# Performance work log

Measured on AMD Instinct MI355X. Metric: run time of the kernel, lower is better.

## Reference

```python
import jax, jax.numpy as jnp
import numpy as np

NUM_HEAD = 16

def setup_inputs() -> dict:
    rk = jax.random.key(0)
    k1, k2, k3, k4, k5 = jax.random.split(rk, 5)
    B, Sq, Skv, D = 4, 2048, 2048, 1024
    return {
        "query": jax.random.normal(k1, (B, Sq, D), dtype=jnp.float32),
        "key":   jax.random.normal(k2, (B, Skv, D), dtype=jnp.float32),
        "value": jax.random.normal(k3, (B, Skv, D), dtype=jnp.float32),
        "W": jax.random.normal(k4, (D, D), dtype=jnp.float32) * (D ** -0.5),
        "b": jax.random.normal(k5, (D,), dtype=jnp.float32) * 0.01,
    }

def reference(query, key, value, W, b):
    B, Sq, D = query.shape
    H = NUM_HEAD
    hd = D // H
    # chunk(num_head, -1) == split last dim into H contiguous heads
    q = query.reshape(B, Sq, H, hd)
    k = key.reshape(B, -1, H, hd)
    v = value.reshape(B, -1, H, hd)
    # scores[b,h,q,k] = (Q_h K_h^T) / sqrt(embedding_dim)  (full dim, per source)
    scores = jnp.einsum('bqhd,bkhd->bhqk', q, k) / jnp.sqrt(jnp.float32(D))
    # nn.Softmax(dim=1) on a [B, q, kv] matrix -> softmax over the QUERY axis
    attn = jax.nn.softmax(scores, axis=2)
    out = jnp.einsum('bhqk,bkhd->bqhd', attn, v).reshape(B, Sq, D)
    # final linear: x @ W^T + b
    return out @ W.T + b
```

## Files before the change

kernel.cpp:

```cpp
#include <hip/hip_runtime.h>

#define NH    16
#define HD    64
#define SQ    2048
#define SKV   2048
#define DM    1024

typedef __attribute__((ext_vector_type(8))) __bf16 bf16x8;
typedef __attribute__((ext_vector_type(4))) __bf16 bf16x4;
typedef __attribute__((ext_vector_type(4))) float  f32x4;

#define ASYNC16(gp, lp)                                                        \
    __builtin_amdgcn_global_load_lds(                                          \
        (const __attribute__((address_space(1))) void*)(gp),                   \
        (__attribute__((address_space(3))) void*)(lp), 16, 0, 0)

#if __has_builtin(__builtin_amdgcn_exp2f)
#define EXPS(x) __builtin_amdgcn_exp2f((x) * 0.04508422f)
#else
#define EXPS(x) __expf((x) * 0.03125f)
#endif

static __device__ __forceinline__ int swz(int row, int chunk) {
    return (row << 6) + (((chunk) ^ (row & 7)) << 3);
}

static __device__ __forceinline__ bf16x4 cvt4(float4 v) {
    bf16x4 r;
    r[0] = (__bf16)v.x; r[1] = (__bf16)v.y; r[2] = (__bf16)v.z; r[3] = (__bf16)v.w;
    return r;
}

__global__ void kprep(const float* __restrict__ src, __bf16* __restrict__ dst) {
    size_t g = (size_t)blockIdx.x * 256 + threadIdx.x;
    size_t o = g * 8;
    int c  = (int)(o & 63);
    int s  = (int)((o >> 6) & 2047);
    int bh = (int)(o >> 17);
    int b = bh >> 4, h = bh & 15;
    const float* p = src + ((size_t)(b * SQ + s)) * DM + h * HD + c;
    float4 v0 = *(const float4*)p;
    float4 v1 = *(const float4*)(p + 4);
    bf16x8 r;
    r[0] = (__bf16)v0.x; r[1] = (__bf16)v0.y; r[2] = (__bf16)v0.z; r[3] = (__bf16)v0.w;
    r[4] = (__bf16)v1.x; r[5] = (__bf16)v1.y; r[6] = (__bf16)v1.z; r[7] = (__bf16)v1.w;
    *(bf16x8*)(dst + o) = r;
}

__global__ void kconv_w(const float* __restrict__ W, __bf16* __restrict__ Wb) {
    int i = blockIdx.x * 256 + threadIdx.x;
    float4 v = *(const float4*)(W + (size_t)i * 4);
    *(bf16x4*)(Wb + (size_t)i * 4) = cvt4(v);
}

__global__ __launch_bounds__(256, 3) void kz(const __bf16* __restrict__ Qh,
                                             const __bf16* __restrict__ Kh,
                                             const float* __restrict__ v,
                                             __bf16* __restrict__ Vt) {
    const int bh = blockIdx.x;
    const int kb = blockIdx.y;
    const int b = bh >> 4, h = bh & 15;
    const int t = threadIdx.x;
    const int w = t >> 6, lane = t & 63;
    const int lo16 = lane & 15, quad = lane >> 4;
    const int wub = (t & 192) << 3;

    __shared__ __bf16 Ks[256 * 64];
    __shared__ __bf16 Qs[64 * 64];
    __shared__ float  Zs[256];

    const __bf16* kbase = Kh + ((size_t)bh * SKV + kb * 256) * HD;
    const __bf16* qbase = Qh + (size_t)bh * SQ * HD;

#pragma unroll
    for (int i = 0; i < 8; ++i) {
        int ci = i * 256 + t;
        int row = ci >> 3;
        int c = (ci & 7) ^ (row & 7);
        ASYNC16(kbase + row * 64 + c * 8, &Ks[i * 2048 + wub]);
    }
    __syncthreads();

    bf16x8 bk[4][2];
#pragma unroll
    for (int nt = 0; nt < 4; ++nt)
#pragma unroll
        for (int dh = 0; dh < 2; ++dh)
            bk[nt][dh] = *(const bf16x8*)(&Ks[swz(w * 64 + nt * 16 + lo16, dh * 4 + quad)]);

    float zacc[4] = {0.f, 0.f, 0.f, 0.f};

    for (int qt = 0; qt < 32; ++qt) {
        __syncthreads();
#pragma unroll
        for (int i = 0; i < 2; ++i) {
            int ci = i * 256 + t;
            int row = ci >> 3;
            int c = (ci & 7) ^ (row & 7);
            ASYNC16(qbase + (size_t)qt * 64 * HD + row * 64 + c * 8, &Qs[i * 2048 + wub]);
        }
        __syncthreads();

#pragma unroll
        for (int mt = 0; mt < 4; ++mt) {
            bf16x8 aq0 = *(const bf16x8*)(&Qs[swz(mt * 16 + lo16, quad)]);
            bf16x8 aq1 = *(const bf16x8*)(&Qs[swz(mt * 16 + lo16, 4 + quad)]);
#pragma unroll
            for (int nt = 0; nt < 4; ++nt) {
                f32x4 acc = {0.f, 0.f, 0.f, 0.f};
                acc = __builtin_amdgcn_mfma_f32_16x16x32_bf16(aq0, bk[nt][0], acc, 0, 0, 0);
                acc = __builtin_amdgcn_mfma_f32_16x16x32_bf16(aq1, bk[nt][1], acc, 0, 0, 0);
                zacc[nt] += EXPS(acc[0]) + EXPS(acc[1]) + EXPS(acc[2]) + EXPS(acc[3]);
            }
        }
    }

#pragma unroll
    for (int nt = 0; nt < 4; ++nt) {
        float s = zacc[nt];
        s += __shfl_xor(s, 16, 64);
        s += __shfl_xor(s, 32, 64);
        if (lane < 16) Zs[w * 64 + nt * 16 + lane] = s;
    }
    __syncthreads();

    {
        float rz = 1.0f / Zs[t];
        const float* vrow = v + ((size_t)(b * SKV) + kb * 256 + t) * DM + h * HD;
        size_t vtb = (size_t)bh * HD * SKV + kb * 256 + t;
#pragma unroll
        for (int dc = 0; dc < 4; ++dc) {
            float4 a0 = *(const float4*)(vrow + dc * 16 + 0);
            float4 a1 = *(const float4*)(vrow + dc * 16 + 4);
            float4 a2 = *(const float4*)(vrow + dc * 16 + 8);
            float4 a3 = *(const float4*)(vrow + dc * 16 + 12);
            float tmp[16] = {a0.x, a0.y, a0.z, a0.w, a1.x, a1.y, a1.z, a1.w,
                             a2.x, a2.y, a2.z, a2.w, a3.x, a3.y, a3.z, a3.w};
#pragma unroll
            for (int j = 0; j < 16; ++j)
                Vt[vtb + (size_t)(dc * 16 + j) * SKV] = (__bf16)(tmp[j] * rz);
        }
    }
}

__global__ __launch_bounds__(256, 3) void kattn(const __bf16* __restrict__ Qh,
                                                const __bf16* __restrict__ Kh,
                                                const __bf16* __restrict__ Vt,
                                                __bf16* __restrict__ O) {
    const int bh = blockIdx.x;
    const int qb = blockIdx.y;
    const int b = bh >> 4, h = bh & 15;
    const int t = threadIdx.x;
    const int w = t >> 6, lane = t & 63;
    const int lo16 = lane & 15, quad = lane >> 4;
    const int wub = (t & 192) << 3;

    __shared__ __bf16 Ks[64 * 64];
    __shared__ __bf16 Vts[64 * 64];
    __shared__ __bf16 QE[256 * 64];

    const __bf16* qgbase = Qh + ((size_t)bh * SQ + qb * 256) * HD;
#pragma unroll
    for (int i = 0; i < 8; ++i) {
        int ci = i * 256 + t;
        int row = ci >> 3;
        int c = (ci & 7) ^ (row & 7);
        ASYNC16(qgbase + row * 64 + c * 8, &QE[i * 2048 + wub]);
    }
    __syncthreads();

    bf16x8 qf[4][2];
#pragma unroll
    for (int qt = 0; qt < 4; ++qt)
#pragma unroll
        for (int dh = 0; dh < 2; ++dh)
            qf[qt][dh] = *(const bf16x8*)(&QE[swz(w * 64 + qt * 16 + lo16, dh * 4 + quad)]);

    f32x4 oacc[4][4];
    f32x4 zero = {0.f, 0.f, 0.f, 0.f};
#pragma unroll
    for (int qt = 0; qt < 4; ++qt)
#pragma unroll
        for (int nt = 0; nt < 4; ++nt)
            oacc[qt][nt] = zero;

    __bf16* Ew = &QE[w * 64 * 64];
    const __bf16* kgbase = Kh + (size_t)bh * SKV * HD;
    const __bf16* vtgbase = Vt + (size_t)bh * HD * SKV;

    for (int kt = 0; kt < 32; ++kt) {
        __syncthreads();
#pragma unroll
        for (int i = 0; i < 2; ++i) {
            int ci = i * 256 + t;
            int row = ci >> 3;
            int c = (ci & 7) ^ (row & 7);
            ASYNC16(kgbase + (size_t)kt * 64 * HD + row * 64 + c * 8, &Ks[i * 2048 + wub]);
            ASYNC16(vtgbase + (size_t)row * SKV + kt * 64 + c * 8, &Vts[i * 2048 + wub]);
        }
        __syncthreads();

#pragma unroll
        for (int ktile = 0; ktile < 4; ++ktile) {
            bf16x8 ak0 = *(const bf16x8*)(&Ks[swz(ktile * 16 + lo16, quad)]);
            bf16x8 ak1 = *(const bf16x8*)(&Ks[swz(ktile * 16 + lo16, 4 + quad)]);
#pragma unroll
            for (int qt = 0; qt < 4; ++qt) {
                f32x4 s = zero;
                s = __builtin_amdgcn_mfma_f32_16x16x32_bf16(ak0, qf[qt][0], s, 0, 0, 0);
                s = __builtin_amdgcn_mfma_f32_16x16x32_bf16(ak1, qf[qt][1], s, 0, 0, 0);
                bf16x4 e;
                e[0] = (__bf16)EXPS(s[0]);
                e[1] = (__bf16)EXPS(s[1]);
                e[2] = (__bf16)EXPS(s[2]);
                e[3] = (__bf16)EXPS(s[3]);
                int er = qt * 16 + lo16;
                *(bf16x4*)(&Ew[(er << 6) + ((((2 * ktile + (quad >> 1))) ^ (er & 7)) << 3)
                               + (quad & 1) * 4]) = e;
            }
        }

#pragma unroll
        for (int kk2 = 0; kk2 < 2; ++kk2) {
            bf16x8 ae[4];
#pragma unroll
            for (int qt = 0; qt < 4; ++qt)
                ae[qt] = *(const bf16x8*)(&Ew[swz(qt * 16 + lo16, kk2 * 4 + quad)]);
#pragma unroll
            for (int nt = 0; nt < 4; ++nt) {
                bf16x8 bv = *(const bf16x8*)(&Vts[swz(nt * 16 + lo16, kk2 * 4 + quad)]);
#pragma unroll
                for (int qt = 0; qt < 4; ++qt)
                    oacc[qt][nt] = __builtin_amdgcn_mfma_f32_16x16x32_bf16(ae[qt], bv, oacc[qt][nt], 0, 0, 0);
            }
        }
    }

    size_t obase = ((size_t)(b * SQ) + qb * 256 + w * 64) * DM + h * HD;
#pragma unroll
    for (int qt = 0; qt < 4; ++qt)
#pragma unroll
        for (int nt = 0; nt < 4; ++nt)
#pragma unroll
            for (int r = 0; r < 4; ++r)
                O[obase + (size_t)(qt * 16 + quad * 4 + r) * DM + nt * 16 + lo16] =
                    (__bf16)oacc[qt][nt][r];
}

__global__ __launch_bounds__(256, 3) void kproj(const __bf16* __restrict__ A,
                                                const __bf16* __restrict__ Wb,
                                                const float* __restrict__ bias,
                                                float* __restrict__ out) {
    const int nb = blockIdx.x;
    const int mb = blockIdx.y;
    const int t = threadIdx.x;
    const int w = t >> 6, lane = t & 63;
    const int lo16 = lane & 15, quad = lane >> 4;
    const int wm = w & 1, wn = w >> 1;
    const int wub = (t & 192) << 3;

    __shared__ __bf16 As[128 * 64];
    __shared__ __bf16 Bs[128 * 64];

    f32x4 acc[4][4];
    f32x4 zero = {0.f, 0.f, 0.f, 0.f};
#pragma unroll
    for (int mt = 0; mt < 4; ++mt)
#pragma unroll
        for (int nt = 0; nt < 4; ++nt)
            acc[mt][nt] = zero;

    const __bf16* abase = A + (size_t)(mb * 128) * DM;
    const __bf16* wbase = Wb + (size_t)(nb * 128) * DM;

    for (int kt = 0; kt < 16; ++kt) {
        __syncthreads();
#pragma unroll
        for (int i = 0; i < 4; ++i) {
            int ci = i * 256 + t;
            int row = ci >> 3;
            int c = (ci & 7) ^ (row & 7);
            ASYNC16(abase + (size_t)row * DM + kt * 64 + c * 8, &As[i * 2048 + wub]);
            ASYNC16(wbase + (size_t)row * DM + kt * 64 + c * 8, &Bs[i * 2048 + wub]);
        }
        __syncthreads();

#pragma unroll
        for (int ks = 0; ks < 2; ++ks) {
            bf16x8 av[4], bv[4];
#pragma unroll
            for (int mt = 0; mt < 4; ++mt)
                av[mt] = *(const bf16x8*)(&As[swz(wm * 64 + mt * 16 + lo16, ks * 4 + quad)]);
#pragma unroll
            for (int nt = 0; nt < 4; ++nt)
                bv[nt] = *(const bf16x8*)(&Bs[swz(wn * 64 + nt * 16 + lo16, ks * 4 + quad)]);
#pragma unroll
            for (int mt = 0; mt < 4; ++mt)
#pragma unroll
                for (int nt = 0; nt < 4; ++nt)
                    acc[mt][nt] = __builtin_amdgcn_mfma_f32_16x16x32_bf16(av[mt], bv[nt], acc[mt][nt], 0, 0, 0);
        }
    }

    const int col0 = nb * 128 + wn * 64;
    const int row0 = mb * 128 + wm * 64;
#pragma unroll
    for (int nt = 0; nt < 4; ++nt) {
        float bb = bias[col0 + nt * 16 + lo16];
#pragma unroll
        for (int mt = 0; mt < 4; ++mt)
#pragma unroll
            for (int r = 0; r < 4; ++r)
                out[(size_t)(row0 + mt * 16 + quad * 4 + r) * DM + col0 + nt * 16 + lo16] =
                    acc[mt][nt][r] + bb;
    }
}

extern "C" void kernel_launch(void* const* d_in, const int* in_sizes, int n_in,
                              void* d_out, int out_size, void* d_ws, size_t ws_size,
                              hipStream_t stream) {
    const float* q    = (const float*)d_in[0];
    const float* k    = (const float*)d_in[1];
    const float* v    = (const float*)d_in[2];
    const float* W    = (const float*)d_in[3];
    const float* bias = (const float*)d_in[4];
    float* out = (float*)d_out;

    char* ws = (char*)d_ws;
    __bf16* Qh = (__bf16*)ws;
    __bf16* Kh = (__bf16*)(ws + (16u << 20));
    __bf16* Vt = (__bf16*)(ws + (32u << 20));
    __bf16* Wb = (__bf16*)(ws + (48u << 20));
    __bf16* O  = (__bf16*)(ws + (50u << 20));

    kprep  <<<dim3(4096), 256, 0, stream>>>(q, Qh);
    kprep  <<<dim3(4096), 256, 0, stream>>>(k, Kh);
    kconv_w<<<dim3(1024), 256, 0, stream>>>(W, Wb);
    kz     <<<dim3(64, 8), 256, 0, stream>>>(Qh, Kh, v, Vt);
    kattn  <<<dim3(64, 8), 256, 0, stream>>>(Qh, Kh, Vt, O);
    kproj  <<<dim3(8, 64), 256, 0, stream>>>(O, Wb, bias, out);
}
```

Before: 298.5 us.

## Double-buffer LDS tiles in attention and projection kernels, merge prep launches

Switches the kz, kattn and kproj main loops from single-buffered LDS tiles to double buffering. The next tile's async global-to-LDS load is issued before computing on the current tile, with one barrier per iteration instead of two. The three conversion kernels are merged into one launch, and launch_bounds occupancy hints drop from 3 to 2 blocks per CU to make room for the larger shared footprint. The risk is lower occupancy, and the overlap depends on the async loads being waited on correctly at the single barrier.

```diff
diff --git a/kernel.cpp b/kernel.cpp
--- a/kernel.cpp
+++ b/kernel.cpp
@@ -31,29 +31,35 @@
     return r;
 }
 
-__global__ void kprep(const float* __restrict__ src, __bf16* __restrict__ dst) {
-    size_t g = (size_t)blockIdx.x * 256 + threadIdx.x;
-    size_t o = g * 8;
-    int c  = (int)(o & 63);
-    int s  = (int)((o >> 6) & 2047);
-    int bh = (int)(o >> 17);
-    int b = bh >> 4, h = bh & 15;
-    const float* p = src + ((size_t)(b * SQ + s)) * DM + h * HD + c;
-    float4 v0 = *(const float4*)p;
-    float4 v1 = *(const float4*)(p + 4);
-    bf16x8 r;
-    r[0] = (__bf16)v0.x; r[1] = (__bf16)v0.y; r[2] = (__bf16)v0.z; r[3] = (__bf16)v0.w;
-    r[4] = (__bf16)v1.x; r[5] = (__bf16)v1.y; r[6] = (__bf16)v1.z; r[7] = (__bf16)v1.w;
-    *(bf16x8*)(dst + o) = r;
-}
-
-__global__ void kconv_w(const float* __restrict__ W, __bf16* __restrict__ Wb) {
-    int i = blockIdx.x * 256 + threadIdx.x;
-    float4 v = *(const float4*)(W + (size_t)i * 4);
-    *(bf16x4*)(Wb + (size_t)i * 4) = cvt4(v);
-}
-
-__global__ __launch_bounds__(256, 3) void kz(const __bf16* __restrict__ Qh,
+__global__ void kprep_all(const float* __restrict__ q, const float* __restrict__ k,
+                          const float* __restrict__ W,
+                          __bf16* __restrict__ Qh, __bf16* __restrict__ Kh,
+                          __bf16* __restrict__ Wb) {
+    int bid = blockIdx.x;
+    if (bid < 8192) {
+        const float* src = (bid < 4096) ? q : k;
+        __bf16* dst = (bid < 4096) ? Qh : Kh;
+        size_t g = (size_t)(bid & 4095) * 256 + threadIdx.x;
+        size_t o = g * 8;
+        int c  = (int)(o & 63);
+        int s  = (int)((o >> 6) & 2047);
+        int bh = (int)(o >> 17);
+        int b = bh >> 4, h = bh & 15;
+        const float* p = src + ((size_t)(b * SQ + s)) * DM + h * HD + c;
+        float4 v0 = *(const float4*)p;
+        float4 v1 = *(const float4*)(p + 4);
+        bf16x8 r;
+        r[0] = (__bf16)v0.x; r[1] = (__bf16)v0.y; r[2] = (__bf16)v0.z; r[3] = (__bf16)v0.w;
+        r[4] = (__bf16)v1.x; r[5] = (__bf16)v1.y; r[6] = (__bf16)v1.z; r[7] = (__bf16)v1.w;
+        *(bf16x8*)(dst + o) = r;
+    } else {
+        int i = (bid - 8192) * 256 + threadIdx.x;
+        float4 v = *(const float4*)(W + (size_t)i * 4);
+        *(bf16x4*)(Wb + (size_t)i * 4) = cvt4(v);
+    }
+}
+
+__global__ __launch_bounds__(256, 2) void kz(const __bf16* __restrict__ Qh,
                                              const __bf16* __restrict__ Kh,
                                              const float* __restrict__ v,
                                              __bf16* __restrict__ Vt) {
@@ -66,7 +72,7 @@
     const int wub = (t & 192) << 3;
 
     __shared__ __bf16 Ks[256 * 64];
-    __shared__ __bf16 Qs[64 * 64];
+    __shared__ __bf16 Qs[2][64 * 64];
     __shared__ float  Zs[256];
 
     const __bf16* kbase = Kh + ((size_t)bh * SKV + kb * 256) * HD;
@@ -79,6 +85,13 @@
         int c = (ci & 7) ^ (row & 7);
         ASYNC16(kbase + row * 64 + c * 8, &Ks[i * 2048 + wub]);
     }
+#pragma unroll
+    for (int i = 0; i < 2; ++i) {
+        int ci = i * 256 + t;
+        int row = ci >> 3;
+        int c = (ci & 7) ^ (row & 7);
+        ASYNC16(qbase + row * 64 + c * 8, &Qs[0][i * 2048 + wub]);
+    }
     __syncthreads();
 
     bf16x8 bk[4][2];
@@ -91,20 +104,22 @@
     float zacc[4] = {0.f, 0.f, 0.f, 0.f};
 
     for (int qt = 0; qt < 32; ++qt) {
-        __syncthreads();
-#pragma unroll
-        for (int i = 0; i < 2; ++i) {
-            int ci = i * 256 + t;
-            int row = ci >> 3;
-            int c = (ci & 7) ^ (row & 7);
-            ASYNC16(qbase + (size_t)qt * 64 * HD + row * 64 + c * 8, &Qs[i * 2048 + wub]);
-        }
-        __syncthreads();
+        const int cur = qt & 1, nxt = cur ^ 1;
+        if (qt < 31) {
+#pragma unroll
+            for (int i = 0; i < 2; ++i) {
+                int ci = i * 256 + t;
+                int row = ci >> 3;
+                int c = (ci & 7) ^ (row & 7);
+                ASYNC16(qbase + (size_t)(qt + 1) * 64 * HD + row * 64 + c * 8,
+                        &Qs[nxt][i * 2048 + wub]);
+            }
+        }
 
 #pragma unroll
         for (int mt = 0; mt < 4; ++mt) {
-            bf16x8 aq0 = *(const bf16x8*)(&Qs[swz(mt * 16 + lo16, quad)]);
-            bf16x8 aq1 = *(const bf16x8*)(&Qs[swz(mt * 16 + lo16, 4 + quad)]);
+            bf16x8 aq0 = *(const bf16x8*)(&Qs[cur][swz(mt * 16 + lo16, quad)]);
+            bf16x8 aq1 = *(const bf16x8*)(&Qs[cur][swz(mt * 16 + lo16, 4 + quad)]);
 #pragma unroll
             for (int nt = 0; nt < 4; ++nt) {
                 f32x4 acc = {0.f, 0.f, 0.f, 0.f};
@@ -113,6 +128,7 @@
                 zacc[nt] += EXPS(acc[0]) + EXPS(acc[1]) + EXPS(acc[2]) + EXPS(acc[3]);
             }
         }
+        __syncthreads();
     }
 
 #pragma unroll
@@ -143,7 +159,7 @@
     }
 }
 
-__global__ __launch_bounds__(256, 3) void kattn(const __bf16* __restrict__ Qh,
+__global__ __launch_bounds__(256, 2) void kattn(const __bf16* __restrict__ Qh,
                                                 const __bf16* __restrict__ Kh,
                                                 const __bf16* __restrict__ Vt,
                                                 __bf16* __restrict__ O) {
@@ -155,17 +171,28 @@
     const int lo16 = lane & 15, quad = lane >> 4;
     const int wub = (t & 192) << 3;
 
-    __shared__ __bf16 Ks[64 * 64];
-    __shared__ __bf16 Vts[64 * 64];
+    __shared__ __bf16 Ks[2][64 * 64];
+    __shared__ __bf16 Vts[2][64 * 64];
     __shared__ __bf16 QE[256 * 64];
 
     const __bf16* qgbase = Qh + ((size_t)bh * SQ + qb * 256) * HD;
+    const __bf16* kgbase = Kh + (size_t)bh * SKV * HD;
+    const __bf16* vtgbase = Vt + (size_t)bh * HD * SKV;
+
 #pragma unroll
     for (int i = 0; i < 8; ++i) {
         int ci = i * 256 + t;
         int row = ci >> 3;
         int c = (ci & 7) ^ (row & 7);
         ASYNC16(qgbase + row * 64 + c * 8, &QE[i * 2048 + wub]);
+    }
+#pragma unroll
+    for (int i = 0; i < 2; ++i) {
+        int ci = i * 256 + t;
+        int row = ci >> 3;
+        int c = (ci & 7) ^ (row & 7);
+        ASYNC16(kgbase + row * 64 + c * 8, &Ks[0][i * 2048 + wub]);
+        ASYNC16(vtgbase + (size_t)row * SKV + c * 8, &Vts[0][i * 2048 + wub]);
     }
     __syncthreads();
 
@@ -185,25 +212,26 @@
             oacc[qt][nt] = zero;
 
     __bf16* Ew = &QE[w * 64 * 64];
-    const __bf16* kgbase = Kh + (size_t)bh * SKV * HD;
-    const __bf16* vtgbase = Vt + (size_t)bh * HD * SKV;
 
     for (int kt = 0; kt < 32; ++kt) {
-        __syncthreads();
-#pragma unroll
-        for (int i = 0; i < 2; ++i) {
-            int ci = i * 256 + t;
-            int row = ci >> 3;
-            int c = (ci & 7) ^ (row & 7);
-            ASYNC16(kgbase + (size_t)kt * 64 * HD + row * 64 + c * 8, &Ks[i * 2048 + wub]);
-            ASYNC16(vtgbase + (size_t)row * SKV + kt * 64 + c * 8, &Vts[i * 2048 + wub]);
-        }
-        __syncthreads();
+        const int cur = kt & 1, nxt = cur ^ 1;
+        if (kt < 31) {
+#pragma unroll
+            for (int i = 0; i < 2; ++i) {
+                int ci = i * 256 + t;
+                int row = ci >> 3;
+                int c = (ci & 7) ^ (row & 7);
+                ASYNC16(kgbase + (size_t)(kt + 1) * 64 * HD + row * 64 + c * 8,
+                        &Ks[nxt][i * 2048 + wub]);
+                ASYNC16(vtgbase + (size_t)row * SKV + (kt + 1) * 64 + c * 8,
+                        &Vts[nxt][i * 2048 + wub]);
+            }
+        }
 
 #pragma unroll
         for (int ktile = 0; ktile < 4; ++ktile) {
-            bf16x8 ak0 = *(const bf16x8*)(&Ks[swz(ktile * 16 + lo16, quad)]);
-            bf16x8 ak1 = *(const bf16x8*)(&Ks[swz(ktile * 16 + lo16, 4 + quad)]);
+            bf16x8 ak0 = *(const bf16x8*)(&Ks[cur][swz(ktile * 16 + lo16, quad)]);
+            bf16x8 ak1 = *(const bf16x8*)(&Ks[cur][swz(ktile * 16 + lo16, 4 + quad)]);
 #pragma unroll
             for (int qt = 0; qt < 4; ++qt) {
                 f32x4 s = zero;
@@ -228,12 +256,13 @@
                 ae[qt] = *(const bf16x8*)(&Ew[swz(qt * 16 + lo16, kk2 * 4 + quad)]);
 #pragma unroll
             for (int nt = 0; nt < 4; ++nt) {
-                bf16x8 bv = *(const bf16x8*)(&Vts[swz(nt * 16 + lo16, kk2 * 4 + quad)]);
+                bf16x8 bv = *(const bf16x8*)(&Vts[cur][swz(nt * 16 + lo16, kk2 * 4 + quad)]);
 #pragma unroll
                 for (int qt = 0; qt < 4; ++qt)
                     oacc[qt][nt] = __builtin_amdgcn_mfma_f32_16x16x32_bf16(ae[qt], bv, oacc[qt][nt], 0, 0, 0);
             }
         }
+        __syncthreads();
     }
 
     size_t obase = ((size_t)(b * SQ) + qb * 256 + w * 64) * DM + h * HD;
@@ -247,7 +276,7 @@
                     (__bf16)oacc[qt][nt][r];
 }
 
-__global__ __launch_bounds__(256, 3) void kproj(const __bf16* __restrict__ A,
+__global__ __launch_bounds__(256, 2) void kproj(const __bf16* __restrict__ A,
                                                 const __bf16* __restrict__ Wb,
                                                 const float* __restrict__ bias,
                                                 float* __restrict__ out) {
@@ -259,8 +288,8 @@
     const int wm = w & 1, wn = w >> 1;
     const int wub = (t & 192) << 3;
 
-    __shared__ __bf16 As[128 * 64];
-    __shared__ __bf16 Bs[128 * 64];
+    __shared__ __bf16 As[2][128 * 64];
+    __shared__ __bf16 Bs[2][128 * 64];
 
     f32x4 acc[4][4];
     f32x4 zero = {0.f, 0.f, 0.f, 0.f};
@@ -273,33 +302,45 @@
     const __bf16* abase = A + (size_t)(mb * 128) * DM;
     const __bf16* wbase = Wb + (size_t)(nb * 128) * DM;
 
+#pragma unroll
+    for (int i = 0; i < 4; ++i) {
+        int ci = i * 256 + t;
+        int row = ci >> 3;
+        int c = (ci & 7) ^ (row & 7);
+        ASYNC16(abase + (size_t)row * DM + c * 8, &As[0][i * 2048 + wub]);
+        ASYNC16(wbase + (size_t)row * DM + c * 8, &Bs[0][i * 2048 + wub]);
+    }
+    __syncthreads();
+
     for (int kt = 0; kt < 16; ++kt) {
-        __syncthreads();
-#pragma unroll
-        for (int i = 0; i < 4; ++i) {
-            int ci = i * 256 + t;
-            int row = ci >> 3;
-            int c = (ci & 7) ^ (row & 7);
-            ASYNC16(abase + (size_t)row * DM + kt * 64 + c * 8, &As[i * 2048 + wub]);
-            ASYNC16(wbase + (size_t)row * DM + kt * 64 + c * 8, &Bs[i * 2048 + wub]);
-        }
-        __syncthreads();
+        const int cur = kt & 1, nxt = cur ^ 1;
+        if (kt < 15) {
+#pragma unroll
+            for (int i = 0; i < 4; ++i) {
+                int ci = i * 256 + t;
+                int row = ci >> 3;
+                int c = (ci & 7) ^ (row & 7);
+                ASYNC16(abase + (size_t)row * DM + (kt + 1) * 64 + c * 8, &As[nxt][i * 2048 + wub]);
+                ASYNC16(wbase + (size_t)row * DM + (kt + 1) * 64 + c * 8, &Bs[nxt][i * 2048 + wub]);
+            }
+        }
 
 #pragma unroll
         for (int ks = 0; ks < 2; ++ks) {
             bf16x8 av[4], bv[4];
 #pragma unroll
             for (int mt = 0; mt < 4; ++mt)
-                av[mt] = *(const bf16x8*)(&As[swz(wm * 64 + mt * 16 + lo16, ks * 4 + quad)]);
+                av[mt] = *(const bf16x8*)(&As[cur][swz(wm * 64 + mt * 16 + lo16, ks * 4 + quad)]);
 #pragma unroll
             for (int nt = 0; nt < 4; ++nt)
-                bv[nt] = *(const bf16x8*)(&Bs[swz(wn * 64 + nt * 16 + lo16, ks * 4 + quad)]);
+                bv[nt] = *(const bf16x8*)(&Bs[cur][swz(wn * 64 + nt * 16 + lo16, ks * 4 + quad)]);
 #pragma unroll
             for (int mt = 0; mt < 4; ++mt)
 #pragma unroll
                 for (int nt = 0; nt < 4; ++nt)
                     acc[mt][nt] = __builtin_amdgcn_mfma_f32_16x16x32_bf16(av[mt], bv[nt], acc[mt][nt], 0, 0, 0);
         }
+        __syncthreads();
     }
 
     const int col0 = nb * 128 + wn * 64;
@@ -333,10 +374,8 @@
     __bf16* Wb = (__bf16*)(ws + (48u << 20));
     __bf16* O  = (__bf16*)(ws + (50u << 20));
 
-    kprep  <<<dim3(4096), 256, 0, stream>>>(q, Qh);
-    kprep  <<<dim3(4096), 256, 0, stream>>>(k, Kh);
-    kconv_w<<<dim3(1024), 256, 0, stream>>>(W, Wb);
-    kz     <<<dim3(64, 8), 256, 0, stream>>>(Qh, Kh, v, Vt);
-    kattn  <<<dim3(64, 8), 256, 0, stream>>>(Qh, Kh, Vt, O);
-    kproj  <<<dim3(8, 64), 256, 0, stream>>>(O, Wb, bias, out);
-}
+    kprep_all<<<dim3(9216), 256, 0, stream>>>(q, k, W, Qh, Kh, Wb);
+    kz       <<<dim3(64, 8), 256, 0, stream>>>(Qh, Kh, v, Vt);
+    kattn    <<<dim3(64, 8), 256, 0, stream>>>(Qh, Kh, Vt, O);
+    kproj    <<<dim3(8, 64), 256, 0, stream>>>(O, Wb, bias, out);
+}
```

Result: no change. 294.4 us (-1.4%).
